# Optimization experiments

Hardware: AMD Instinct MI355X
Metric: run time of the kernel (lower is better)

Reference implementation:

```python
import jax, jax.numpy as jnp
import numpy as np

N_NODES = 50000
N_EDGES = 800000
IN_DIM = 512
OUT_DIM = 512


def setup_inputs() -> dict:
    key = jax.random.key(0)
    ks = jax.random.split(key, 8)
    x = jax.random.normal(ks[0], (N_NODES, IN_DIM), dtype=jnp.float32)
    edge_index = jax.random.randint(ks[1], (2, N_EDGES), 0, N_NODES, dtype=jnp.int64)
    s = 1.0 / np.sqrt(IN_DIM)
    # SAGEConv params: lin_l (applied to aggregated neighbors, with bias),
    # lin_r (applied to root/self features, no bias). Two convs: loc and scale.
    Wl1 = jax.random.uniform(ks[2], (OUT_DIM, IN_DIM), jnp.float32, -s, s)
    bl1 = jnp.zeros((OUT_DIM,), jnp.float32)
    Wr1 = jax.random.uniform(ks[3], (OUT_DIM, IN_DIM), jnp.float32, -s, s)
    Wl2 = jax.random.uniform(ks[4], (OUT_DIM, IN_DIM), jnp.float32, -s, s)
    bl2 = jnp.zeros((OUT_DIM,), jnp.float32)
    Wr2 = jax.random.uniform(ks[5], (OUT_DIM, IN_DIM), jnp.float32, -s, s)
    return {"x": x, "edge_index": edge_index,
            "Wl1": Wl1, "bl1": bl1, "Wr1": Wr1,
            "Wl2": Wl2, "bl2": bl2, "Wr2": Wr2}


def _sage_conv(x, agg, Wl, bl, Wr):
    # lin_l(sum-aggregated neighbors) + lin_r(x)
    return agg @ Wl.T + bl + x @ Wr.T


def reference(x, edge_index, Wl1, bl1, Wr1, Wl2, bl2, Wr2):
    src, dst = edge_index[0], edge_index[1]
    # sum aggregation of source features into destination nodes: [N, in_dim]
    agg = jax.ops.segment_sum(x[src], dst, num_segments=N_NODES)
    loc = _sage_conv(x, agg, Wl1, bl1, Wr1)
    loc = jnp.clip(loc, -100.0, 100.0)
    scale = jax.nn.softplus(_sage_conv(x, agg, Wl2, bl2, Wr2)) + 0.001
    scale = jnp.minimum(scale, 100.0)
    return (loc, scale)
```

## Files before the change

### kernel.cpp

```cpp
#include <hip/hip_runtime.h>
#include <stdint.h>

#define N_NODES 50000
#define N_EDGES 800000
#define IN_DIM 512
#define OUT_DIM 512
#define KDIM 1024
#define NDIM 1024

typedef __bf16 bf16x8 __attribute__((ext_vector_type(8)));
typedef float f32x4 __attribute__((ext_vector_type(4)));

__device__ __forceinline__ unsigned short f2bf(float f) {
    union { float f; unsigned u; } c; c.f = f;
    unsigned u = c.u;
    u += 0x7fffu + ((u >> 16) & 1u);
    return (unsigned short)(u >> 16);
}
__device__ __forceinline__ float bf2f(unsigned short h) {
    union { unsigned u; float f; } c; c.u = ((unsigned)h) << 16;
    return c.f;
}

#define XCONV_BLOCKS ((N_NODES * IN_DIM / 4 + 255) / 256)
#define COUNT_BLOCKS ((N_EDGES + 255) / 256)
#define WCONV_BLOCKS ((NDIM * KDIM + 255) / 256)

__global__ __launch_bounds__(256) void prep_kernel(
    const float* __restrict__ x, unsigned short* __restrict__ xb,
    const int* __restrict__ ei, int* __restrict__ counts,
    const float* __restrict__ Wl1, const float* __restrict__ Wr1,
    const float* __restrict__ Wl2, const float* __restrict__ Wr2,
    unsigned short* __restrict__ Wb) {
    int b = blockIdx.x;
    if (b < XCONV_BLOCKS) {
        int i = b * 256 + threadIdx.x;
        const int n4 = N_NODES * IN_DIM / 4;
        if (i < n4) {
            float4 v = ((const float4*)x)[i];
            ushort4 o;
            o.x = f2bf(v.x); o.y = f2bf(v.y); o.z = f2bf(v.z); o.w = f2bf(v.w);
            ((ushort4*)xb)[i] = o;
        }
    } else if (b < XCONV_BLOCKS + COUNT_BLOCKS) {
        int i = (b - XCONV_BLOCKS) * 256 + threadIdx.x;
        if (i < N_EDGES) {
            int dst = ei[N_EDGES + i];
            dst = min(max(dst, 0), N_NODES - 1);
            atomicAdd(&counts[dst], 1);
        }
    } else {
        int i = (b - XCONV_BLOCKS - COUNT_BLOCKS) * 256 + threadIdx.x;
        if (i < NDIM * KDIM) {
            int n = i >> 10, k = i & 1023;
            const float* src;
            if (n < 512) src = (k < 512) ? Wl1 : Wr1;
            else         src = (k < 512) ? Wl2 : Wr2;
            int nn = n & 511, kk = k & 511;
            Wb[i] = f2bf(src[nn * 512 + kk]);
        }
    }
}

__global__ __launch_bounds__(1024) void scan_local_kernel(
    const int* __restrict__ cnt, int* __restrict__ offs,
    int* __restrict__ bsums, int n) {
    __shared__ int warp_sums[16];
    int tid = threadIdx.x;
    int lane = tid & 63;
    int w = tid >> 6;
    int i = blockIdx.x * 1024 + tid;
    int v = (i < n) ? cnt[i] : 0;
    int s = v;
    #pragma unroll
    for (int d = 1; d < 64; d <<= 1) {
        int t = __shfl_up(s, d, 64);
        if (lane >= d) s += t;
    }
    if (lane == 63) warp_sums[w] = s;
    __syncthreads();
    if (w == 0) {
        int ws = (lane < 16) ? warp_sums[lane] : 0;
        #pragma unroll
        for (int d = 1; d < 16; d <<= 1) {
            int t = __shfl_up(ws, d, 64);
            if (lane >= d) ws += t;
        }
        if (lane < 16) warp_sums[lane] = ws;
    }
    __syncthreads();
    int base = (w > 0 ? warp_sums[w - 1] : 0);
    if (i < n) offs[i] = base + s - v;
    if (tid == 1023) bsums[blockIdx.x] = base + s;
}

__global__ __launch_bounds__(1024) void scan_apply_kernel(
    int* __restrict__ offs, int* __restrict__ cursor,
    const int* __restrict__ bsums, const int* __restrict__ cnt, int n) {
    __shared__ int s_base;
    int tid = threadIdx.x;
    if (tid < 64) {
        int v = (tid < (int)blockIdx.x) ? bsums[tid] : 0;
        #pragma unroll
        for (int d = 32; d > 0; d >>= 1) v += __shfl_down(v, d, 64);
        if (tid == 0) s_base = v;
    }
    __syncthreads();
    int i = blockIdx.x * 1024 + tid;
    if (i < n) {
        int o = offs[i] + s_base;
        offs[i] = o;
        cursor[i] = o;
        if (i == n - 1) offs[n] = o + cnt[i];
    }
}

__global__ void fill_kernel(const int* __restrict__ ei, int* __restrict__ cursor,
                            int* __restrict__ bucket) {
    int i = blockIdx.x * blockDim.x + threadIdx.x;
    if (i < N_EDGES) {
        int src = ei[i];
        int dst = ei[N_EDGES + i];
        src = min(max(src, 0), N_NODES - 1);
        dst = min(max(dst, 0), N_NODES - 1);
        int pos = atomicAdd(&cursor[dst], 1);
        bucket[pos] = src;
    }
}

__global__ __launch_bounds__(256) void aggregate_kernel(
    const unsigned short* __restrict__ xb, const int* __restrict__ offs,
    const int* __restrict__ bucket, unsigned short* __restrict__ aggb) {
    int wid = threadIdx.x >> 6;
    int lane = threadIdx.x & 63;
    int n = blockIdx.x * 4 + wid;
    if (n >= N_NODES) return;
    int beg = offs[n], end = offs[n + 1];
    float a0[8] = {}, a1[8] = {};
    int e = beg;
    for (; e + 8 <= end; e += 8) {
        int idx[8];
        #pragma unroll
        for (int u = 0; u < 8; ++u) idx[u] = bucket[e + u];
        uint4 v[8];
        #pragma unroll
        for (int u = 0; u < 8; ++u) v[u] = *(const uint4*)(xb + (size_t)idx[u] * IN_DIM + lane * 8);
        #pragma unroll
        for (int u = 0; u < 8; ++u) {
            float* a = (u & 1) ? a1 : a0;
            a[0] += bf2f((unsigned short)(v[u].x & 0xffffu)); a[1] += bf2f((unsigned short)(v[u].x >> 16));
            a[2] += bf2f((unsigned short)(v[u].y & 0xffffu)); a[3] += bf2f((unsigned short)(v[u].y >> 16));
            a[4] += bf2f((unsigned short)(v[u].z & 0xffffu)); a[5] += bf2f((unsigned short)(v[u].z >> 16));
            a[6] += bf2f((unsigned short)(v[u].w & 0xffffu)); a[7] += bf2f((unsigned short)(v[u].w >> 16));
        }
    }
    for (; e < end; ++e) {
        int s = bucket[e];
        uint4 v = *(const uint4*)(xb + (size_t)s * IN_DIM + lane * 8);
        a0[0] += bf2f((unsigned short)(v.x & 0xffffu)); a0[1] += bf2f((unsigned short)(v.x >> 16));
        a0[2] += bf2f((unsigned short)(v.y & 0xffffu)); a0[3] += bf2f((unsigned short)(v.y >> 16));
        a0[4] += bf2f((unsigned short)(v.z & 0xffffu)); a0[5] += bf2f((unsigned short)(v.z >> 16));
        a0[6] += bf2f((unsigned short)(v.w & 0xffffu)); a0[7] += bf2f((unsigned short)(v.w >> 16));
    }
    uint4 o;
    o.x = (unsigned)f2bf(a0[0] + a1[0]) | ((unsigned)f2bf(a0[1] + a1[1]) << 16);
    o.y = (unsigned)f2bf(a0[2] + a1[2]) | ((unsigned)f2bf(a0[3] + a1[3]) << 16);
    o.z = (unsigned)f2bf(a0[4] + a1[4]) | ((unsigned)f2bf(a0[5] + a1[5]) << 16);
    o.w = (unsigned)f2bf(a0[6] + a1[6]) | ((unsigned)f2bf(a0[7] + a1[7]) << 16);
    *(uint4*)(aggb + (size_t)n * IN_DIM + lane * 8) = o;
}

#define BM 128
#define BN 128
#define BK 64
#define NT_TILES (NDIM / BN)
#define MT_TILES ((N_NODES + BM - 1) / BM)
#define NWG (NT_TILES * MT_TILES)
#define NKT (KDIM / BK)

__device__ __forceinline__ void async_copy16(const void* g, void* lds) {
    __builtin_amdgcn_global_load_lds((const __attribute__((address_space(1))) void*)g,
                                     (__attribute__((address_space(3))) void*)lds, 16, 0, 0);
}

__global__ __launch_bounds__(256, 2) void gemm_kernel(
    const unsigned short* __restrict__ aggb,
    const unsigned short* __restrict__ xb,
    const unsigned short* __restrict__ Wb,
    const float* __restrict__ bl1, const float* __restrict__ bl2,
    float* __restrict__ out) {
    constexpr int M = N_NODES;
    __shared__ unsigned short sA[2][BM * BK];
    __shared__ unsigned short sB[2][BN * BK];

    int bid = blockIdx.x;
    int logical = (bid & 7) * (NWG / 8) + (bid >> 3);
    int nt = logical & (NT_TILES - 1);
    int mt = logical >> 3;
    int n0 = nt * BN;
    int m0 = mt * BM;

    int tid = threadIdx.x;
    int lane = tid & 63;
    int w = tid >> 6;
    int wm = (w >> 1) * 64, wn = (w & 1) * 64;

    f32x4 acc[4][4] = {};

    int fr = lane & 15, q = lane >> 4;
    int sl0 = ((q ^ (fr & 7)) << 3);
    int sl1 = (((q + 4) ^ (fr & 7)) << 3);

    auto STAGE = [&](int t, int buf) {
        if (t >= NKT) return;
        int kk = t * BK;
        const unsigned short* Asrc = (kk < 512) ? aggb : xb;
        int ak = kk & 511;
        #pragma unroll
        for (int iss = 0; iss < 4; ++iss) {
            int C = iss * 256 + tid;
            int r = C >> 3, p = C & 7;
            int gr = m0 + r; if (gr >= M) gr = M - 1;
            const unsigned short* g = Asrc + (size_t)gr * 512 + ak + ((p ^ (r & 7)) << 3);
            async_copy16(g, &sA[buf][(size_t)(iss * 256 + (tid & ~63)) * 8]);
        }
        #pragma unroll
        for (int iss = 0; iss < 4; ++iss) {
            int C = iss * 256 + tid;
            int r = C >> 3, p = C & 7;
            const unsigned short* g = Wb + (size_t)(n0 + r) * KDIM + kk + ((p ^ (r & 7)) << 3);
            async_copy16(g, &sB[buf][(size_t)(iss * 256 + (tid & ~63)) * 8]);
        }
    };
    auto COMPUTE = [&](int buf) {
        #pragma unroll
        for (int ksub = 0; ksub < 2; ++ksub) {
            int sl = ksub ? sl1 : sl0;
            bf16x8 af[4], bfg[4];
            #pragma unroll
            for (int i = 0; i < 4; ++i)
                af[i] = *(const bf16x8*)(&sA[buf][0] + (wm + i * 16 + fr) * BK + sl);
            #pragma unroll
            for (int j = 0; j < 4; ++j)
                bfg[j] = *(const bf16x8*)(&sB[buf][0] + (wn + j * 16 + fr) * BK + sl);
            #pragma unroll
            for (int i = 0; i < 4; ++i)
                #pragma unroll
                for (int j = 0; j < 4; ++j)
                    acc[i][j] = __builtin_amdgcn_mfma_f32_16x16x32_bf16(af[i], bfg[j], acc[i][j], 0, 0, 0);
        }
    };

    STAGE(0, 0);
    __syncthreads();
    for (int t = 0; t < NKT; t += 2) {
        STAGE(t + 1, 1);
        COMPUTE(0);
        __syncthreads();
        STAGE(t + 2, 0);
        COMPUTE(1);
        __syncthreads();
    }

    bool is_scale = (n0 >= 512);
    const float* bias = is_scale ? bl2 : bl1;
    float* obase = out + (is_scale ? (size_t)N_NODES * OUT_DIM : 0);
    int ncol0 = is_scale ? (n0 - 512) : n0;
    int rq = lane >> 4;
    #pragma unroll
    for (int i = 0; i < 4; ++i) {
        #pragma unroll
        for (int j = 0; j < 4; ++j) {
            int colg = ncol0 + wn + j * 16 + fr;
            float b = bias[colg];
            #pragma unroll
            for (int r = 0; r < 4; ++r) {
                int rowg = m0 + wm + i * 16 + rq * 4 + r;
                if (rowg < M) {
                    float v = acc[i][j][r] + b;
                    float res;
                    if (is_scale) {
                        float sp = fmaxf(v, 0.f) + __logf(1.f + __expf(-fabsf(v)));
                        res = fminf(sp + 0.001f, 100.f);
                    } else {
                        res = fminf(fmaxf(v, -100.f), 100.f);
                    }
                    __builtin_nontemporal_store(res, &obase[(size_t)rowg * OUT_DIM + colg]);
                }
            }
        }
    }
}

extern "C" void kernel_launch(void* const* d_in, const int* in_sizes, int n_in,
                              void* d_out, int out_size, void* d_ws, size_t ws_size,
                              hipStream_t stream) {
    const float* x       = (const float*)d_in[0];
    const int* ei        = (const int*)d_in[1];
    const float* Wl1     = (const float*)d_in[2];
    const float* bl1     = (const float*)d_in[3];
    const float* Wr1     = (const float*)d_in[4];
    const float* Wl2     = (const float*)d_in[5];
    const float* bl2     = (const float*)d_in[6];
    const float* Wr2     = (const float*)d_in[7];
    float* out = (float*)d_out;

    char* ws = (char*)d_ws;
    size_t off = 0;
    auto alloc = [&](size_t bytes) -> void* {
        void* p = ws + off;
        off = (off + bytes + 255) & ~(size_t)255;
        return p;
    };
    unsigned short* xb    = (unsigned short*)alloc((size_t)N_NODES * IN_DIM * 2);
    unsigned short* aggb  = (unsigned short*)alloc((size_t)N_NODES * IN_DIM * 2);
    unsigned short* Wb    = (unsigned short*)alloc((size_t)NDIM * KDIM * 2);
    int* counts           = (int*)alloc((size_t)(N_NODES + 1) * 4);
    int* offs             = (int*)alloc((size_t)(N_NODES + 1) * 4);
    int* cursor           = (int*)alloc((size_t)N_NODES * 4);
    int* bucket           = (int*)alloc((size_t)N_EDGES * 4);
    int* bsums            = (int*)alloc(64 * 4);

    hipMemsetAsync(counts, 0, (size_t)(N_NODES + 1) * 4, stream);

    const int nb = (N_NODES + 1023) / 1024;

    prep_kernel<<<XCONV_BLOCKS + COUNT_BLOCKS + WCONV_BLOCKS, 256, 0, stream>>>(
        x, xb, ei, counts, Wl1, Wr1, Wl2, Wr2, Wb);
    scan_local_kernel<<<nb, 1024, 0, stream>>>(counts, offs, bsums, N_NODES);
    scan_apply_kernel<<<nb, 1024, 0, stream>>>(offs, cursor, bsums, counts, N_NODES);
    fill_kernel<<<(N_EDGES + 255) / 256, 256, 0, stream>>>(ei, cursor, bucket);
    aggregate_kernel<<<(N_NODES + 3) / 4, 256, 0, stream>>>(xb, offs, bucket, aggb);

    gemm_kernel<<<NWG, 256, 0, stream>>>(aggb, xb, Wb, bl1, bl2, out);
}
```

Measured before the change: 622.8 us.

## Replace double-buffered LDS pipeline with single-buffer load-sync-compute loop

The GEMM kernel drops its two-stage LDS double buffering and moves to a single buffer, where each K step loads a tile, synchronizes, computes, then synchronizes again. This halves LDS use per block, which could let more blocks run per CU. In exchange, global-to-LDS copies no longer overlap with MFMA compute, which exposes memory latency on every K step.

```diff
diff --git a/kernel.cpp b/kernel.cpp
--- a/kernel.cpp
+++ b/kernel.cpp
@@ -176,7 +176,6 @@
 #define NT_TILES (NDIM / BN)
 #define MT_TILES ((N_NODES + BM - 1) / BM)
 #define NWG (NT_TILES * MT_TILES)
-#define NKT (KDIM / BK)
 
 __device__ __forceinline__ void async_copy16(const void* g, void* lds) {
     __builtin_amdgcn_global_load_lds((const __attribute__((address_space(1))) void*)g,
@@ -190,8 +189,8 @@
     const float* __restrict__ bl1, const float* __restrict__ bl2,
     float* __restrict__ out) {
     constexpr int M = N_NODES;
-    __shared__ unsigned short sA[2][BM * BK];
-    __shared__ unsigned short sB[2][BN * BK];
+    __shared__ unsigned short sA[BM * BK];
+    __shared__ unsigned short sB[BN * BK];
 
     int bid = blockIdx.x;
     int logical = (bid & 7) * (NWG / 8) + (bid >> 3);
@@ -211,54 +210,43 @@
     int sl0 = ((q ^ (fr & 7)) << 3);
     int sl1 = (((q + 4) ^ (fr & 7)) << 3);
 
-    auto STAGE = [&](int t, int buf) {
-        if (t >= NKT) return;
-        int kk = t * BK;
-        const unsigned short* Asrc = (kk < 512) ? aggb : xb;
-        int ak = kk & 511;
+    for (int k0 = 0; k0 < KDIM; k0 += BK) {
+        const unsigned short* Asrc;
+        int ak;
+        if (k0 < 512) { Asrc = aggb; ak = k0; } else { Asrc = xb; ak = k0 - 512; }
         #pragma unroll
         for (int iss = 0; iss < 4; ++iss) {
             int C = iss * 256 + tid;
             int r = C >> 3, p = C & 7;
             int gr = m0 + r; if (gr >= M) gr = M - 1;
             const unsigned short* g = Asrc + (size_t)gr * 512 + ak + ((p ^ (r & 7)) << 3);
-            async_copy16(g, &sA[buf][(size_t)(iss * 256 + (tid & ~63)) * 8]);
+            async_copy16(g, sA + (size_t)(iss * 256 + w * 64) * 8);
         }
         #pragma unroll
         for (int iss = 0; iss < 4; ++iss) {
             int C = iss * 256 + tid;
             int r = C >> 3, p = C & 7;
-            const unsigned short* g = Wb + (size_t)(n0 + r) * KDIM + kk + ((p ^ (r & 7)) << 3);
-            async_copy16(g, &sB[buf][(size_t)(iss * 256 + (tid & ~63)) * 8]);
-        }
-    };
-    auto COMPUTE = [&](int buf) {
+            const unsigned short* g = Wb + (size_t)(n0 + r) * KDIM + k0 + ((p ^ (r & 7)) << 3);
+            async_copy16(g, sB + (size_t)(iss * 256 + w * 64) * 8);
+        }
+        __syncthreads();
+
         #pragma unroll
         for (int ksub = 0; ksub < 2; ++ksub) {
             int sl = ksub ? sl1 : sl0;
             bf16x8 af[4], bfg[4];
             #pragma unroll
             for (int i = 0; i < 4; ++i)
-                af[i] = *(const bf16x8*)(&sA[buf][0] + (wm + i * 16 + fr) * BK + sl);
+                af[i] = *(const bf16x8*)(sA + (wm + i * 16 + fr) * BK + sl);
             #pragma unroll
             for (int j = 0; j < 4; ++j)
-                bfg[j] = *(const bf16x8*)(&sB[buf][0] + (wn + j * 16 + fr) * BK + sl);
+                bfg[j] = *(const bf16x8*)(sB + (wn + j * 16 + fr) * BK + sl);
             #pragma unroll
             for (int i = 0; i < 4; ++i)
                 #pragma unroll
                 for (int j = 0; j < 4; ++j)
                     acc[i][j] = __builtin_amdgcn_mfma_f32_16x16x32_bf16(af[i], bfg[j], acc[i][j], 0, 0, 0);
         }
-    };
-
-    STAGE(0, 0);
-    __syncthreads();
-    for (int t = 0; t < NKT; t += 2) {
-        STAGE(t + 1, 1);
-        COMPUTE(0);
-        __syncthreads();
-        STAGE(t + 2, 0);
-        COMPUTE(1);
         __syncthreads();
     }
 
```

Measured after the change: 578.4 us. 7.1% less time.
